# Kernel optimization log

Measured on AMD Instinct MI355X. Metric: run time of the kernel, lower is better.

Reference implementation:

```python
import jax, jax.numpy as jnp
import numpy as np

NH, NP, MA, FL = 8, 4, 2, 3   # heads, points, max_num_agent, feature_level
L = MA * FL                    # total sampling levels = 6
C = 256
BS, NQ = 8, 4096
SS = np.array([[64, 64], [32, 32], [16, 16]] * MA, dtype=np.int64)  # [L,2] (H,W)
NV = int((SS[:, 0] * SS[:, 1]).sum())  # 10752


def setup_inputs() -> dict:
    key = jax.random.key(0)
    ks = jax.random.split(key, 8)
    f32 = jnp.float32
    return {
        'query': jax.random.normal(ks[0], (BS, NQ, C), f32),
        'query_pos': jax.random.normal(ks[1], (BS, NQ, C), f32),
        'value': jax.random.normal(ks[2], (BS, NV, C), f32),
        'reference_points': jax.random.uniform(ks[3], (BS, NQ, L, 2), f32),
        'spatial_shapes': SS,
        'W_off': jax.random.normal(ks[4], (C, L * NH * NP * 2), f32) * 0.01,
        'b_off': jnp.zeros((L * NH * NP * 2,), f32),
        'W_attn': jax.random.normal(ks[5], (C, L * NH * NP), f32) * 0.05,
        'b_attn': jnp.zeros((L * NH * NP,), f32),
        'W_val': jax.random.normal(ks[6], (C, C), f32) * 0.05,
        'b_val': jnp.zeros((C,), f32),
        'W_out': jax.random.normal(ks[7], (C, C), f32) * 0.05,
        'b_out': jnp.zeros((C,), f32),
    }


def _ms_deform_attn(v, loc, attn, ss):
    # v: [bs, nv, NH, d]; loc: [bs, nq, NH, L, NP, 2] in [0,1] (x,y)
    # attn: [bs, nq, NH, L, NP]; ss: np int array [L,2] (H,W) -- static
    bs, nq = loc.shape[0], loc.shape[1]
    d = v.shape[-1]
    starts = np.concatenate([[0], np.cumsum(ss[:, 0] * ss[:, 1])[:-1]])
    out = jnp.zeros((bs, NH, nq, d), v.dtype)
    for l in range(L):
        H, W = int(ss[l, 0]), int(ss[l, 1])
        s0 = int(starts[l])
        vl = v[:, s0:s0 + H * W].transpose(0, 2, 1, 3)  # [bs, NH, HW, d]
        # sampling coords, grid_sample align_corners=False convention
        x = loc[:, :, :, l, :, 0].transpose(0, 2, 1, 3) * W - 0.5  # [bs,NH,nq,NP]
        y = loc[:, :, :, l, :, 1].transpose(0, 2, 1, 3) * H - 0.5
        x0 = jnp.floor(x); y0 = jnp.floor(y)
        lx = x - x0; ly = y - y0
        x0i = x0.astype(jnp.int32); y0i = y0.astype(jnp.int32)

        def gather(yi, xi):
            valid = (yi >= 0) & (yi < H) & (xi >= 0) & (xi < W)
            idx = jnp.clip(yi, 0, H - 1) * W + jnp.clip(xi, 0, W - 1)  # [bs,NH,nq,NP]
            g = jnp.take_along_axis(vl, idx.reshape(bs, NH, nq * NP, 1), axis=2)
            g = g.reshape(bs, NH, nq, NP, d)
            return g * valid[..., None].astype(g.dtype)  # zero padding outside

        sampled = ((1 - lx) * (1 - ly))[..., None] * gather(y0i, x0i) \
                + (lx * (1 - ly))[..., None] * gather(y0i, x0i + 1) \
                + ((1 - lx) * ly)[..., None] * gather(y0i + 1, x0i) \
                + (lx * ly)[..., None] * gather(y0i + 1, x0i + 1)
        aw = attn[:, :, :, l, :].transpose(0, 2, 1, 3)  # [bs,NH,nq,NP]
        out = out + jnp.einsum('bhqpd,bhqp->bhqd', sampled, aw)
    return out.transpose(0, 2, 1, 3).reshape(bs, nq, NH * d)


def reference(query, query_pos, value, reference_points, spatial_shapes,
              W_off, b_off, W_attn, b_attn, W_val, b_val, W_out, b_out):
    ss = np.asarray(spatial_shapes)
    identity = query
    q = query + query_pos
    bs, nv, c = value.shape
    nq = q.shape[1]
    v = (value @ W_val + b_val).reshape(bs, nv, NH, c // NH)
    off = (q @ W_off + b_off).reshape(bs, nq, NH, L, NP, 2)
    attn = (q @ W_attn + b_attn).reshape(bs, nq, NH, L * NP)
    attn = jax.nn.softmax(attn, axis=-1).reshape(bs, nq, NH, L, NP)
    offset_normalizer = jnp.asarray(np.stack([ss[:, 1], ss[:, 0]], -1), q.dtype)  # [L,2] (W,H)
    loc = reference_points[:, :, None, :, None, :] \
        + off / offset_normalizer[None, None, None, :, None, :]
    out = _ms_deform_attn(v, loc, attn, ss)
    out = out @ W_out + b_out
    return out + identity  # dropout is identity in eval mode
```

## Files before the change

kernel.cpp:

```cpp
#include <hip/hip_runtime.h>

#define NHEAD 8
#define NPOINT 4
#define NLVL 6
#define CDIM 256
#define BSZ 8
#define NQRY 4096
#define NVAL 10752

typedef __attribute__((ext_vector_type(8))) short short8;
typedef __attribute__((ext_vector_type(4))) float floatx4;

__device__ __forceinline__ unsigned short f2bf(float f) {
    unsigned u = __float_as_uint(f);
    return (unsigned short)((u + 0x7FFFu + ((u >> 16) & 1u)) >> 16);
}
__device__ __forceinline__ unsigned pack2(float a, float b) {
    return (unsigned)f2bf(a) | ((unsigned)f2bf(b) << 16);
}
__device__ __forceinline__ float blo(unsigned u) { return __uint_as_float(u << 16); }
__device__ __forceinline__ float bhi(unsigned u) { return __uint_as_float(u & 0xffff0000u); }

__global__ __launch_bounds__(256) void prep_w(
    const float* __restrict__ Wv, const float* __restrict__ Woff,
    const float* __restrict__ Wattn, const float* __restrict__ Wo,
    unsigned short* __restrict__ Wt)
{
    const int id = blockIdx.x * 256 + threadIdx.x;
    const int n = id >> 8, k = id & 255;
    float val;
    if (n < 256) val = Wv[k * 256 + n];
    else if (n < 832) {
        const int nn = n - 256;
        val = (nn < 384) ? Woff[k * 384 + nn] : Wattn[k * 192 + (nn - 384)];
    } else val = Wo[k * 256 + (n - 832)];
    Wt[id] = f2bf(val);
}

__global__ __launch_bounds__(256) void q_conv(
    const float* __restrict__ query, const float* __restrict__ qpos,
    unsigned short* __restrict__ qbf)
{
    const long i = ((long)blockIdx.x * 256 + threadIdx.x) * 4;
    const float4 a = *(const float4*)(query + i);
    const float4 b = *(const float4*)(qpos + i);
    ushort4 r;
    r.x = f2bf(a.x + b.x); r.y = f2bf(a.y + b.y);
    r.z = f2bf(a.z + b.z); r.w = f2bf(a.w + b.w);
    *(ushort4*)(qbf + i) = r;
}

template<int BN, int ABF, int VTRANS, int RESID, int SPLITB>
__global__ __launch_bounds__(512) void gemm_mfma(
    const void* __restrict__ Av, const unsigned short* __restrict__ Bt,
    const float* __restrict__ bias, const float* __restrict__ bias2,
    const float* __restrict__ resid, void* __restrict__ Cv,
    int M, int Ntot)
{
    constexpr int BK = 32, BMt = 128, PAD = 8;
    constexpr int WN = BN / 4, NT = WN / 16;
    __shared__ unsigned short As[BMt][BK + PAD];
    __shared__ unsigned short Bs[BN][BK + PAD];
    const int tid = threadIdx.x;
    const int bm = blockIdx.y * BMt;
    const int bcol = blockIdx.x * BN;
    const int wid = tid >> 6, lane = tid & 63;
    const int wm = (wid >> 2) * 64, wn = (wid & 3) * WN;
    const int lm = lane & 15, q8 = (lane >> 4) * 8;

    floatx4 acc[4][NT];
#pragma unroll
    for (int i = 0; i < 4; ++i)
#pragma unroll
        for (int j = 0; j < NT; ++j) acc[i][j] = (floatx4)0.0f;

    const int arow = tid >> 2, akp = (tid & 3) * 8;
    const int bn_ = tid >> 1, bkp = (tid & 1) * 16;

    for (int k0 = 0; k0 < 256; k0 += BK) {
        if (ABF) {
            const unsigned short* A = (const unsigned short*)Av;
            uint4 v = *(const uint4*)(A + (long)(bm + arow) * 256 + k0 + akp);
            *(uint4*)&As[arow][akp] = v;
        } else {
            const float* A = (const float*)Av;
            const float* p = A + (long)(bm + arow) * 256 + k0 + akp;
            const float4 a = *(const float4*)p;
            const float4 b = *(const float4*)(p + 4);
            uint4 v;
            v.x = pack2(a.x, a.y); v.y = pack2(a.z, a.w);
            v.z = pack2(b.x, b.y); v.w = pack2(b.z, b.w);
            *(uint4*)&As[arow][akp] = v;
        }
        if (bn_ < BN) {
            const unsigned short* p = Bt + (long)(bcol + bn_) * 256 + k0 + bkp;
            uint4 v0 = *(const uint4*)p;
            uint4 v1 = *(const uint4*)(p + 8);
            *(uint4*)&Bs[bn_][bkp] = v0;
            *(uint4*)&Bs[bn_][bkp + 8] = v1;
        }
        __syncthreads();
        short8 af[4], bfr[NT];
#pragma unroll
        for (int i = 0; i < 4; ++i) af[i] = *(const short8*)&As[wm + i * 16 + lm][q8];
#pragma unroll
        for (int j = 0; j < NT; ++j) bfr[j] = *(const short8*)&Bs[wn + j * 16 + lm][q8];
#pragma unroll
        for (int i = 0; i < 4; ++i)
#pragma unroll
            for (int j = 0; j < NT; ++j)
                acc[i][j] = __builtin_amdgcn_mfma_f32_16x16x32_bf16(af[i], bfr[j], acc[i][j], 0, 0, 0);
        __syncthreads();
    }

    const int qrow = (lane >> 4) * 4;
#pragma unroll
    for (int j = 0; j < NT; ++j) {
        const int colg = bcol + wn + j * 16 + lm;
        const float bv = (SPLITB && colg >= 384) ? bias2[colg - 384] : bias[colg];
#pragma unroll
        for (int i = 0; i < 4; ++i) {
#pragma unroll
            for (int r = 0; r < 4; ++r) {
                const int rowl = wm + i * 16 + qrow + r;
                const int rowg = bm + rowl;
                float val = acc[i][j][r] + bv;
                if (VTRANS) {
                    const int b = bm / NVAL;
                    const int pos = bm - b * NVAL + rowl;
                    const int h = colg >> 5, d = colg & 31;
                    ((unsigned short*)Cv)[(((long)(b * NHEAD + h)) * NVAL + pos) * 32 + d] = f2bf(val);
                } else {
                    if (RESID) val += resid[(long)rowg * 256 + colg];
                    ((float*)Cv)[(long)rowg * Ntot + colg] = val;
                }
            }
        }
    }
}

__global__ __launch_bounds__(256) void ms_sample4(
    const unsigned short* __restrict__ v,
    const float* __restrict__ oa,
    const float* __restrict__ refp,
    unsigned short* __restrict__ outi)
{
    __shared__ float s_oa[4][576];
    __shared__ float s_ref[4][12];
    const int tid = threadIdx.x;
    const int w = tid >> 6;
    const int lane = tid & 63;
    const int bq = blockIdx.x * 4 + w;
    const int b = bq >> 12;

    {
        const float* src = oa + (long)bq * 576;
#pragma unroll
        for (int i = 0; i < 9; ++i) s_oa[w][lane + i * 64] = src[lane + i * 64];
        if (lane < 12) s_ref[w][lane] = refp[(long)bq * 12 + lane];
    }
    __syncthreads();

    const int h = lane >> 3;
    float* sat = &s_oa[w][384 + h * 24];
    float mx = sat[0];
#pragma unroll
    for (int i = 1; i < 24; ++i) mx = fmaxf(mx, sat[i]);
    float den = 0.f;
#pragma unroll
    for (int i = 0; i < 24; ++i) den += __expf(sat[i] - mx);
    const float inv = 1.0f / den;
    {
        const int li = lane & 7;
#pragma unroll
        for (int k = 0; k < 3; ++k) {
            const int i = li * 3 + k;
            sat[i] = __expf(sat[i] - mx) * inv;
        }
    }

    const unsigned short* vb = v + ((long)(b * NHEAD + h)) * NVAL * 32 + (lane & 7) * 4;
    float4 acc = {0.f, 0.f, 0.f, 0.f};

#pragma unroll 2
    for (int lp = 0; lp < NLVL * NPOINT; ++lp) {
        const int l = lp >> 2;
        const int sh = (l >= 3) ? (l - 3) : l;
        const int W = 64 >> sh;
        const int base = ((l >= 3) ? 5376 : 0)
                       + ((sh >= 1) ? 4096 : 0)
                       + ((sh >= 2) ? 1024 : 0);
        const float Wf = (float)W;
        const float aw = sat[lp];
        const float ox = s_oa[w][(h * 24 + lp) * 2 + 0];
        const float oy = s_oa[w][(h * 24 + lp) * 2 + 1];
        const float rx = s_ref[w][l * 2 + 0];
        const float ry = s_ref[w][l * 2 + 1];
        const float x = rx * Wf + ox - 0.5f;
        const float y = ry * Wf + oy - 0.5f;
        const float xf = floorf(x), yf = floorf(y);
        const int x0 = (int)xf, y0 = (int)yf;
        const float lx = x - xf, ly = y - yf;
        const float wx0 = (x0 >= 0 && x0 < W)      ? (1.f - lx) : 0.f;
        const float wx1 = (x0 >= -1 && x0 < W - 1) ? lx         : 0.f;
        const float wy0 = (y0 >= 0 && y0 < W)      ? (1.f - ly) : 0.f;
        const float wy1 = (y0 >= -1 && y0 < W - 1) ? ly         : 0.f;
        const int x0c = min(max(x0, 0), W - 1);
        const int x1c = min(max(x0 + 1, 0), W - 1);
        const int y0c = min(max(y0, 0), W - 1);
        const int y1c = min(max(y0 + 1, 0), W - 1);
        const unsigned short* vl = vb + (long)base * 32;
        const uint2 u00 = *(const uint2*)(vl + (long)(y0c * W + x0c) * 32);
        const uint2 u01 = *(const uint2*)(vl + (long)(y0c * W + x1c) * 32);
        const uint2 u10 = *(const uint2*)(vl + (long)(y1c * W + x0c) * 32);
        const uint2 u11 = *(const uint2*)(vl + (long)(y1c * W + x1c) * 32);
        const float w00 = aw * wx0 * wy0;
        const float w01 = aw * wx1 * wy0;
        const float w10 = aw * wx0 * wy1;
        const float w11 = aw * wx1 * wy1;
        acc.x += w00 * blo(u00.x) + w01 * blo(u01.x) + w10 * blo(u10.x) + w11 * blo(u11.x);
        acc.y += w00 * bhi(u00.x) + w01 * bhi(u01.x) + w10 * bhi(u10.x) + w11 * bhi(u11.x);
        acc.z += w00 * blo(u00.y) + w01 * blo(u01.y) + w10 * blo(u10.y) + w11 * blo(u11.y);
        acc.w += w00 * bhi(u00.y) + w01 * bhi(u01.y) + w10 * bhi(u10.y) + w11 * bhi(u11.y);
    }
    ushort4 o;
    o.x = f2bf(acc.x); o.y = f2bf(acc.y); o.z = f2bf(acc.z); o.w = f2bf(acc.w);
    *(ushort4*)(outi + (long)bq * CDIM + lane * 4) = o;
}

extern "C" void kernel_launch(void* const* d_in, const int* in_sizes, int n_in,
                              void* d_out, int out_size, void* d_ws, size_t ws_size,
                              hipStream_t stream) {
    const float* query     = (const float*)d_in[0];
    const float* query_pos = (const float*)d_in[1];
    const float* value     = (const float*)d_in[2];
    const float* refp      = (const float*)d_in[3];
    const float* W_off  = (const float*)d_in[5];
    const float* b_off  = (const float*)d_in[6];
    const float* W_attn = (const float*)d_in[7];
    const float* b_attn = (const float*)d_in[8];
    const float* W_val  = (const float*)d_in[9];
    const float* b_val  = (const float*)d_in[10];
    const float* W_out  = (const float*)d_in[11];
    const float* b_out  = (const float*)d_in[12];
    float* out = (float*)d_out;

    unsigned short* v_bf = (unsigned short*)d_ws;
    unsigned short* q_bf = v_bf + (long)86016 * 256;
    unsigned short* Wt   = q_bf + (long)32768 * 256;
    float* oa_ws = (float*)(Wt + (long)1088 * 256);
    unsigned short* i_bf = (unsigned short*)(oa_ws + (long)32768 * 576);

    const int MV = BSZ * NVAL;
    const int MQ = BSZ * NQRY;

    prep_w<<<1088, 256, 0, stream>>>(W_val, W_off, W_attn, W_out, Wt);
    q_conv<<<(MQ * CDIM / 4) / 256, 256, 0, stream>>>(query, query_pos, q_bf);
    gemm_mfma<256, 0, 1, 0, 0><<<dim3(1, MV / 128), 512, 0, stream>>>(
        value, Wt, b_val, nullptr, nullptr, v_bf, MV, 256);
    gemm_mfma<192, 1, 0, 0, 1><<<dim3(3, MQ / 128), 512, 0, stream>>>(
        q_bf, Wt + (long)256 * 256, b_off, b_attn, nullptr, oa_ws, MQ, 576);
    ms_sample4<<<MQ / 4, 256, 0, stream>>>(v_bf, oa_ws, refp, i_bf);
    gemm_mfma<256, 1, 0, 1, 0><<<dim3(1, MQ / 128), 512, 0, stream>>>(
        i_bf, Wt + (long)832 * 256, b_out, nullptr, query, out, MQ, 256);
}
```

Measured before the change: 411.8 us.

## Split sampling coordinate math across lanes and share via LDS records

In the sampling kernel, each lane now computes the bilinear weights and packed corner indices for only 3 of the 24 (level,point) pairs of its head. The results go to shared memory as compact records, replacing the old scheme where all 8 lanes of a head redundantly computed all 24. Softmax is done with register shuffles instead of shared-memory loops, and the offset/logit staging through LDS is dropped in favour of direct global loads. The gather loop then reads the precomputed weights and 16-bit indices and uses packed float2 FMAs. This adds a second barrier and assumes per-level indices fit in 16 bits.

```diff
diff --git a/kernel.cpp b/kernel.cpp
--- a/kernel.cpp
+++ b/kernel.cpp
@@ -10,6 +10,7 @@
 
 typedef __attribute__((ext_vector_type(8))) short short8;
 typedef __attribute__((ext_vector_type(4))) float floatx4;
+typedef __attribute__((ext_vector_type(2))) float float2v;
 
 __device__ __forceinline__ unsigned short f2bf(float f) {
     unsigned u = __float_as_uint(f);
@@ -145,7 +146,7 @@
     const float* __restrict__ refp,
     unsigned short* __restrict__ outi)
 {
-    __shared__ float s_oa[4][576];
+    __shared__ float s_rec[4][192 * 6];
     __shared__ float s_ref[4][12];
     const int tid = threadIdx.x;
     const int w = tid >> 6;
@@ -153,37 +154,37 @@
     const int bq = blockIdx.x * 4 + w;
     const int b = bq >> 12;
 
-    {
-        const float* src = oa + (long)bq * 576;
-#pragma unroll
-        for (int i = 0; i < 9; ++i) s_oa[w][lane + i * 64] = src[lane + i * 64];
-        if (lane < 12) s_ref[w][lane] = refp[(long)bq * 12 + lane];
-    }
+    if (lane < 12) s_ref[w][lane] = refp[(long)bq * 12 + lane];
     __syncthreads();
 
     const int h = lane >> 3;
-    float* sat = &s_oa[w][384 + h * 24];
-    float mx = sat[0];
-#pragma unroll
-    for (int i = 1; i < 24; ++i) mx = fmaxf(mx, sat[i]);
-    float den = 0.f;
-#pragma unroll
-    for (int i = 0; i < 24; ++i) den += __expf(sat[i] - mx);
+    const int li = lane & 7;
+    const float* oarow = oa + (long)bq * 576;
+
+    const float* lgp = oarow + 384 + h * 24 + li * 3;
+    const float lg0 = lgp[0], lg1 = lgp[1], lg2 = lgp[2];
+    float mx = fmaxf(lg0, fmaxf(lg1, lg2));
+    mx = fmaxf(mx, __shfl_xor(mx, 1));
+    mx = fmaxf(mx, __shfl_xor(mx, 2));
+    mx = fmaxf(mx, __shfl_xor(mx, 4));
+    const float e0 = __expf(lg0 - mx);
+    const float e1 = __expf(lg1 - mx);
+    const float e2 = __expf(lg2 - mx);
+    float den = e0 + e1 + e2;
+    den += __shfl_xor(den, 1);
+    den += __shfl_xor(den, 2);
+    den += __shfl_xor(den, 4);
     const float inv = 1.0f / den;
-    {
-        const int li = lane & 7;
-#pragma unroll
-        for (int k = 0; k < 3; ++k) {
-            const int i = li * 3 + k;
-            sat[i] = __expf(sat[i] - mx) * inv;
-        }
-    }
-
-    const unsigned short* vb = v + ((long)(b * NHEAD + h)) * NVAL * 32 + (lane & 7) * 4;
-    float4 acc = {0.f, 0.f, 0.f, 0.f};
-
-#pragma unroll 2
-    for (int lp = 0; lp < NLVL * NPOINT; ++lp) {
+    const float aw_[3] = {e0 * inv, e1 * inv, e2 * inv};
+
+    const float* offp = oarow + (h * 24 + li * 3) * 2;
+    const float2v od0 = *(const float2v*)(offp);
+    const float2v od1 = *(const float2v*)(offp + 2);
+    const float2v od2 = *(const float2v*)(offp + 4);
+
+#pragma unroll
+    for (int k = 0; k < 3; ++k) {
+        const int lp = li * 3 + k;
         const int l = lp >> 2;
         const int sh = (l >= 3) ? (l - 3) : l;
         const int W = 64 >> sh;
@@ -191,9 +192,8 @@
                        + ((sh >= 1) ? 4096 : 0)
                        + ((sh >= 2) ? 1024 : 0);
         const float Wf = (float)W;
-        const float aw = sat[lp];
-        const float ox = s_oa[w][(h * 24 + lp) * 2 + 0];
-        const float oy = s_oa[w][(h * 24 + lp) * 2 + 1];
+        const float ox = (k == 0) ? od0.x : (k == 1) ? od1.x : od2.x;
+        const float oy = (k == 0) ? od0.y : (k == 1) ? od1.y : od2.y;
         const float rx = s_ref[w][l * 2 + 0];
         const float ry = s_ref[w][l * 2 + 1];
         const float x = rx * Wf + ox - 0.5f;
@@ -209,22 +209,52 @@
         const int x1c = min(max(x0 + 1, 0), W - 1);
         const int y0c = min(max(y0, 0), W - 1);
         const int y1c = min(max(y0 + 1, 0), W - 1);
-        const unsigned short* vl = vb + (long)base * 32;
-        const uint2 u00 = *(const uint2*)(vl + (long)(y0c * W + x0c) * 32);
-        const uint2 u01 = *(const uint2*)(vl + (long)(y0c * W + x1c) * 32);
-        const uint2 u10 = *(const uint2*)(vl + (long)(y1c * W + x0c) * 32);
-        const uint2 u11 = *(const uint2*)(vl + (long)(y1c * W + x1c) * 32);
-        const float w00 = aw * wx0 * wy0;
-        const float w01 = aw * wx1 * wy0;
-        const float w10 = aw * wx0 * wy1;
-        const float w11 = aw * wx1 * wy1;
-        acc.x += w00 * blo(u00.x) + w01 * blo(u01.x) + w10 * blo(u10.x) + w11 * blo(u11.x);
-        acc.y += w00 * bhi(u00.x) + w01 * bhi(u01.x) + w10 * bhi(u10.x) + w11 * bhi(u11.x);
-        acc.z += w00 * blo(u00.y) + w01 * blo(u01.y) + w10 * blo(u10.y) + w11 * blo(u11.y);
-        acc.w += w00 * bhi(u00.y) + w01 * bhi(u01.y) + w10 * bhi(u10.y) + w11 * bhi(u11.y);
+        const float aw = aw_[k];
+        const unsigned p00 = (unsigned)(base + y0c * W + x0c);
+        const unsigned p01 = (unsigned)(base + y0c * W + x1c);
+        const unsigned p10 = (unsigned)(base + y1c * W + x0c);
+        const unsigned p11 = (unsigned)(base + y1c * W + x1c);
+        float* r = &s_rec[w][((lp << 3) + h) * 6];
+        float2v wa, wb;
+        wa.x = aw * wx0 * wy0; wa.y = aw * wx1 * wy0;
+        wb.x = aw * wx0 * wy1; wb.y = aw * wx1 * wy1;
+        *(float2v*)(r)     = wa;
+        *(float2v*)(r + 2) = wb;
+        uint2 pk;
+        pk.x = p00 | (p01 << 16);
+        pk.y = p10 | (p11 << 16);
+        *(uint2*)(r + 4) = pk;
+    }
+    __syncthreads();
+
+    const unsigned short* vb = v + ((long)(b * NHEAD + h)) * NVAL * 32 + li * 4;
+    float2v acc01 = {0.f, 0.f};
+    float2v acc23 = {0.f, 0.f};
+    const float* rp0 = &s_rec[w][h * 6];
+
+#pragma unroll 4
+    for (int lp = 0; lp < NLVL * NPOINT; ++lp) {
+        const float* rp = rp0 + lp * 48;
+        const float2v w01 = *(const float2v*)(rp);
+        const float2v w23 = *(const float2v*)(rp + 2);
+        const uint2 pp = *(const uint2*)(rp + 4);
+        const uint2 u00 = *(const uint2*)(vb + ((pp.x & 0xffffu) << 5));
+        const uint2 u01 = *(const uint2*)(vb + ((pp.x >> 16) << 5));
+        const uint2 u10 = *(const uint2*)(vb + ((pp.y & 0xffffu) << 5));
+        const uint2 u11 = *(const uint2*)(vb + ((pp.y >> 16) << 5));
+        float2v c;
+        c.x = blo(u00.x); c.y = bhi(u00.x); acc01 += w01.x * c;
+        c.x = blo(u00.y); c.y = bhi(u00.y); acc23 += w01.x * c;
+        c.x = blo(u01.x); c.y = bhi(u01.x); acc01 += w01.y * c;
+        c.x = blo(u01.y); c.y = bhi(u01.y); acc23 += w01.y * c;
+        c.x = blo(u10.x); c.y = bhi(u10.x); acc01 += w23.x * c;
+        c.x = blo(u10.y); c.y = bhi(u10.y); acc23 += w23.x * c;
+        c.x = blo(u11.x); c.y = bhi(u11.x); acc01 += w23.y * c;
+        c.x = blo(u11.y); c.y = bhi(u11.y); acc23 += w23.y * c;
     }
     ushort4 o;
-    o.x = f2bf(acc.x); o.y = f2bf(acc.y); o.z = f2bf(acc.z); o.w = f2bf(acc.w);
+    o.x = f2bf(acc01.x); o.y = f2bf(acc01.y);
+    o.z = f2bf(acc23.x); o.w = f2bf(acc23.y);
     *(ushort4*)(outi + (long)bq * CDIM + lane * 4) = o;
 }
 
```

After: 399.0 us. 1.03x faster.
